# Kernel optimization log

Hardware: AMD Instinct MI355X
Metric: run time of the kernel (lower is better)

The kernel has to match this reference:

```python
import math
import jax, jax.numpy as jnp
import numpy as np

D_MODEL = 768
EXPAND = 2
D_INNER = EXPAND * D_MODEL  # 1536
D_STATE = 16
D_CONV = 4
DT_RANK = math.ceil(D_INNER / 16)  # 96
B, L = 2, 2048
LN_EPS = 1e-5


def setup_inputs() -> dict:
    key = jax.random.key(0)
    ks = jax.random.split(key, 10)
    x = jax.random.normal(ks[0], (B, L, D_MODEL), dtype=jnp.float32)
    ln_g = jnp.ones((D_MODEL,), jnp.float32)
    ln_b = jnp.zeros((D_MODEL,), jnp.float32)
    W_in = jax.random.normal(ks[1], (D_MODEL, 2 * D_INNER), jnp.float32) / np.sqrt(D_MODEL)
    conv_w = jax.random.normal(ks[2], (D_INNER, 1, D_CONV), jnp.float32) / np.sqrt(D_CONV)
    conv_b = jax.random.normal(ks[3], (D_INNER,), jnp.float32) * 0.02
    W_xproj = jax.random.normal(ks[4], (D_INNER, DT_RANK + 2 * D_STATE), jnp.float32) / np.sqrt(D_INNER)
    W_dt = jax.random.normal(ks[5], (DT_RANK, D_INNER), jnp.float32) / np.sqrt(DT_RANK)
    # dt bias init: inverse-softplus of dt ~ LogUniform(1e-3, 1e-1)
    dt = jnp.exp(jax.random.uniform(ks[6], (D_INNER,)) * (math.log(0.1) - math.log(0.001)) + math.log(0.001))
    b_dt = dt + jnp.log(-jnp.expm1(-dt))
    log_A = jnp.log(jnp.tile(jnp.arange(1, D_STATE + 1, dtype=jnp.float32), (D_INNER, 1)))  # (d_inner, N)
    D_param = jnp.ones((D_INNER,), jnp.float32)
    W_out = jax.random.normal(ks[7], (D_INNER, D_MODEL), jnp.float32) / np.sqrt(D_INNER)
    return dict(x=x, ln_g=ln_g, ln_b=ln_b, W_in=W_in, conv_w=conv_w, conv_b=conv_b,
                W_xproj=W_xproj, W_dt=W_dt, b_dt=b_dt, log_A=log_A, D_param=D_param, W_out=W_out)


def _mamba_block(x, ln_g, ln_b, W_in, conv_w, conv_b, W_xproj, W_dt, b_dt, log_A, D_param, W_out):
    residual = x
    # LayerNorm
    mu = jnp.mean(x, axis=-1, keepdims=True)
    var = jnp.var(x, axis=-1, keepdims=True)
    xn = (x - mu) * jax.lax.rsqrt(var + LN_EPS) * ln_g + ln_b
    # in projection -> (u, v)
    uv = xn @ W_in  # (B, L, 2*d_inner)
    u, v = jnp.split(uv, 2, axis=-1)
    # causal depthwise conv1d along length (torch pads both sides then truncates -> left pad only)
    u_c = jnp.transpose(u, (0, 2, 1))  # (B, d_inner, L)
    u_c = jax.lax.conv_general_dilated(
        u_c, conv_w, window_strides=(1,), padding=[(D_CONV - 1, 0)],
        dimension_numbers=('NCH', 'OIH', 'NCH'), feature_group_count=D_INNER)
    u_c = u_c + conv_b[None, :, None]
    u = jnp.transpose(u_c, (0, 2, 1))  # (B, L, d_inner)
    u = jax.nn.silu(u)
    # Selective SSM
    x_dbl = u @ W_xproj  # (B, L, dt_rank + 2N)
    dlt, Bm, Cm = jnp.split(x_dbl, [DT_RANK, DT_RANK + D_STATE], axis=-1)
    delta = jax.nn.softplus(dlt @ W_dt + b_dt)  # (B, L, d_inner)
    A = -jnp.exp(log_A)  # (d_inner, N)
    A_bar = jnp.exp(jnp.einsum('bld,dn->bldn', delta, A))         # discretized A
    Bu = jnp.einsum('bld,bln,bld->bldn', delta, Bm, u)            # B_bar * u
    # parallel scan: h_k = A_bar_k * h_{k-1} + Bu_k
    def comb(e1, e2):
        a1, b1 = e1
        a2, b2 = e2
        return a1 * a2, a2 * b1 + b2
    _, h = jax.lax.associative_scan(comb, (A_bar, Bu), axis=1)
    y = jnp.einsum('bldn,bln->bld', h, Cm) + u * D_param
    # gate + residual
    y = y * jax.nn.silu(v)
    return y @ W_out + residual


def reference(x, ln_g, ln_b, W_in, conv_w, conv_b, W_xproj, W_dt, b_dt, log_A, D_param, W_out):
    return _mamba_block(x, ln_g, ln_b, W_in, conv_w, conv_b, W_xproj, W_dt, b_dt, log_A, D_param, W_out)
```

## Files before the change

kernel.cpp:

```cpp
#include <hip/hip_runtime.h>

#define D_MODEL 768
#define D_INNER 1536
#define D_STATE 16
#define DT_RANK 96
#define BB 2
#define LL 2048
#define TT (BB*LL)
#define NC 64
#define CL 32
#define SKK 4
#define LOG2E 1.44269504f

typedef unsigned short u16;
typedef short bf16x8 __attribute__((ext_vector_type(8)));
typedef unsigned short u16x8 __attribute__((ext_vector_type(8)));
typedef float f32x4  __attribute__((ext_vector_type(4)));

__device__ __forceinline__ float bf2f(u16 u) {
    union { unsigned int i; float f; } c; c.i = ((unsigned int)u) << 16; return c.f;
}
__device__ __forceinline__ u16 f2bf(float f) {
    union { float f; unsigned int i; } c; c.f = f;
    unsigned int x = c.i;
    return (u16)((x + 0x7fffu + ((x >> 16) & 1u)) >> 16);
}
__device__ __forceinline__ float bfu_lo(unsigned int u) {
    union { unsigned int i; float f; } c; c.i = u << 16; return c.f;
}
__device__ __forceinline__ float bfu_hi(unsigned int u) {
    union { unsigned int i; float f; } c; c.i = u & 0xFFFF0000u; return c.f;
}
__device__ __forceinline__ float ldx(const void* p, size_t i, bool f32) {
    return f32 ? ((const float*)p)[i] : bf2f(((const u16*)p)[i]);
}

__device__ __forceinline__ void gload16(const u16* g, u16* l) {
    __builtin_amdgcn_global_load_lds(
        (const __attribute__((address_space(1))) unsigned int*)g,
        (__attribute__((address_space(3))) unsigned int*)l, 16, 0, 0);
}

__device__ __forceinline__ void xcd_swz(int& bx, int& by) {
    const int gx = gridDim.x;
    const int cpx = (gx * gridDim.y) >> 3;
    const int bid = by * gx + bx;
    const int w = (bid & 7) * cpx + (bid >> 3);
    bx = w % gx; by = w / gx;
}

__global__ __launch_bounds__(256) void prep_kernel(
    const void* __restrict__ W_in, const void* __restrict__ W_xp,
    const void* __restrict__ W_dt, const void* __restrict__ W_out,
    u16* __restrict__ WtIn, u16* __restrict__ WtXp,
    u16* __restrict__ WtDt, u16* __restrict__ WtOut,
    const void* __restrict__ x, const void* __restrict__ g,
    const void* __restrict__ b, u16* __restrict__ xn,
    int* __restrict__ flagw)
{
    const int t = threadIdx.x;
    __shared__ int sbad;
    if (t == 0) sbad = 0;
    __syncthreads();
    {
        const u16* px = (const u16*)x;
        int bad = 0;
        for (int i = t; i < 2048; i += 256)
            if (!(fabsf(bf2f(px[2 * i])) < 1e4f)) bad = 1;
        if (bad) atomicOr(&sbad, 1);
    }
    __syncthreads();
    const bool f32 = (sbad != 0);
    int bid = blockIdx.x;
    if (bid == 0 && t == 0) *flagw = sbad;
    if (bid >= 960) {
        const int tok = bid - 960;
        const size_t base = (size_t)tok * D_MODEL;
        float v[3];
        v[0] = ldx(x, base + t, f32);
        v[1] = ldx(x, base + t + 256, f32);
        v[2] = ldx(x, base + t + 512, f32);
        float s = v[0] + v[1] + v[2];
        float q = v[0]*v[0] + v[1]*v[1] + v[2]*v[2];
        #pragma unroll
        for (int o = 32; o > 0; o >>= 1) {
            s += __shfl_down(s, o, 64);
            q += __shfl_down(q, o, 64);
        }
        __shared__ float ss[4], qq[4];
        if ((t & 63) == 0) { ss[t >> 6] = s; qq[t >> 6] = q; }
        __syncthreads();
        const float S = ss[0] + ss[1] + ss[2] + ss[3];
        const float Q = qq[0] + qq[1] + qq[2] + qq[3];
        const float mu  = S * (1.f / D_MODEL);
        const float var = Q * (1.f / D_MODEL) - mu * mu;
        const float rs  = rsqrtf(var + 1e-5f);
        u16* outr = xn + base;
        #pragma unroll
        for (int i = 0; i < 3; ++i) {
            const int c = t + i * 256;
            outr[c] = f2bf((v[i] - mu) * rs * ldx(g, c, f32) + ldx(b, c, f32));
        }
        return;
    }
    const void* src; u16* dst; int K, N, bx, by;
    if (bid < 576)      { src = W_in;  dst = WtIn;  K = 768;  N = 3072; bx = bid % 48; by = bid / 48; }
    else if (bid < 624) { bid -= 576; src = W_xp;  dst = WtXp;  K = 1536; N = 128;  bx = bid % 2;  by = bid / 2; }
    else if (bid < 672) { bid -= 624; src = W_dt;  dst = WtDt;  K = 96;   N = 1536; bx = bid % 24; by = bid / 24; }
    else                { bid -= 672; src = W_out; dst = WtOut; K = 1536; N = 768;  bx = bid % 12; by = bid / 12; }
    __shared__ u16 tile[64][72];
    const int n0 = bx * 64, k0 = by * 64;
    {
        const int r = t >> 2, c = (t & 3) * 16;
        const int k = k0 + r;
        if (k < K) {
            if (f32) {
                const float* sp = (const float*)src + (size_t)k * N + n0 + c;
                #pragma unroll
                for (int q = 0; q < 4; ++q) {
                    const float4 v = *(const float4*)(sp + 4 * q);
                    tile[r][c + 4*q + 0] = f2bf(v.x);
                    tile[r][c + 4*q + 1] = f2bf(v.y);
                    tile[r][c + 4*q + 2] = f2bf(v.z);
                    tile[r][c + 4*q + 3] = f2bf(v.w);
                }
            } else {
                const u16* sp = (const u16*)src + (size_t)k * N + n0 + c;
                *(u16x8*)(&tile[r][c])     = *(const u16x8*)(sp);
                *(u16x8*)(&tile[r][c + 8]) = *(const u16x8*)(sp + 8);
            }
        }
    }
    __syncthreads();
    {
        const int nl = t >> 2, kl = (t & 3) * 16;
        const int n = n0 + nl;
        if (k0 + kl < K) {
            u16x8 t0, t1;
            #pragma unroll
            for (int i = 0; i < 8; ++i) t0[i] = tile[kl + i][nl];
            #pragma unroll
            for (int i = 0; i < 8; ++i) t1[i] = tile[kl + 8 + i][nl];
            u16* dp = dst + (size_t)n * K + k0 + kl;
            *(u16x8*)(dp)     = t0;
            *(u16x8*)(dp + 8) = t1;
        }
    }
}

template<int EPI, int BK>
__global__ __launch_bounds__(256) void mfma_gemm(
    const u16* __restrict__ A, const u16* __restrict__ Bt,
    u16* __restrict__ C, void* __restrict__ Cout, const void* __restrict__ aux,
    float* __restrict__ Cf, const int* __restrict__ flagp,
    int Kslice, int lda, int ldbt, int ldc)
{
    const bool f32 = (*flagp != 0);
    __shared__ alignas(16) u16 As[3 * 64 * BK];
    __shared__ alignas(16) u16 Bs[3 * 64 * BK];
    const int tid  = threadIdx.x;
    const int wave = tid >> 6, lane = tid & 63;
    const int lrow = lane & 15, quad = lane >> 4;
    int bx = blockIdx.x, by = blockIdx.y;
    if (gridDim.z == 1) xcd_swz(bx, by);
    const int row0 = by * 64, col0 = bx * 64;
    const int k0   = blockIdx.z * Kslice;
    constexpr int LPR = BK / 8;
    constexpr int PM  = LPR - 1;
    constexpr int RPO = 64 / LPR;
    constexpr int NOP = BK / 32;
    constexpr int V1  = 2 * NOP;
    constexpr int V2  = 4 * NOP;
    const int srow = lane / LPR;
    const int pc   = (lane % LPR) ^ (srow & PM);
    const int skk  = pc * 8;
    const int wb   = wave * 16 * BK;
    const u16* gA = A  + (size_t)(row0 + wave * 16 + srow) * lda  + k0 + skk;
    const u16* gB = Bt + (size_t)(col0 + wave * 16 + srow) * ldbt + k0 + skk;
    const int nst = Kslice / BK;
    constexpr int BUF = 64 * BK;
    #pragma unroll
    for (int o = 0; o < NOP; ++o) {
        gload16(gA + (size_t)o * RPO * lda,  &As[wb + o * 512]);
        gload16(gB + (size_t)o * RPO * ldbt, &Bs[wb + o * 512]);
    }
    if (nst > 1) {
        #pragma unroll
        for (int o = 0; o < NOP; ++o) {
            gload16(gA + BK + (size_t)o * RPO * lda,  &As[BUF + wb + o * 512]);
            gload16(gB + BK + (size_t)o * RPO * ldbt, &Bs[BUF + wb + o * 512]);
        }
    }
    f32x4 acc[4] = {{0.f,0.f,0.f,0.f},{0.f,0.f,0.f,0.f},{0.f,0.f,0.f,0.f},{0.f,0.f,0.f,0.f}};
    const int sw = (lrow & PM) << 3;
    int cur = 0, nxt2 = 2;
    for (int t = 0; t < nst; ++t) {
        if (t + 2 < nst) {
            const int kt = (t + 2) * BK;
            const int poff = nxt2 * BUF;
            #pragma unroll
            for (int o = 0; o < NOP; ++o) {
                gload16(gA + kt + (size_t)o * RPO * lda,  &As[poff + wb + o * 512]);
                gload16(gB + kt + (size_t)o * RPO * ldbt, &Bs[poff + wb + o * 512]);
            }
            asm volatile("s_waitcnt vmcnt(%0)" :: "i"(V2) : "memory");
        } else if (t + 1 < nst) {
            asm volatile("s_waitcnt vmcnt(%0)" :: "i"(V1) : "memory");
        } else {
            asm volatile("s_waitcnt vmcnt(0)" ::: "memory");
        }
        __builtin_amdgcn_s_barrier();
        asm volatile("" ::: "memory");
        const int boff = cur * BUF;
        #pragma unroll
        for (int kk = 0; kk < NOP; ++kk) {
            const bf16x8 af = *(const bf16x8*)(
                &As[boff + (wave * 16 + lrow) * BK + ((kk * 32 + quad * 8) ^ sw)]);
            #pragma unroll
            for (int q = 0; q < 4; ++q) {
                const bf16x8 bq = *(const bf16x8*)(
                    &Bs[boff + (q * 16 + lrow) * BK + ((kk * 32 + quad * 8) ^ sw)]);
                acc[q] = __builtin_amdgcn_mfma_f32_16x16x32_bf16(af, bq, acc[q], 0, 0, 0);
            }
        }
        __builtin_amdgcn_s_barrier();
        asm volatile("" ::: "memory");
        cur = (cur == 2) ? 0 : cur + 1;
        nxt2 = (nxt2 == 2) ? 0 : nxt2 + 1;
    }
    #pragma unroll
    for (int t = 0; t < 4; ++t) {
        #pragma unroll
        for (int r = 0; r < 4; ++r) {
            const int row = row0 + wave * 16 + quad * 4 + r;
            const int col = col0 + t * 16 + lrow;
            const size_t idx = (size_t)row * ldc + col;
            float vv = acc[t][r];
            if (EPI == 1) {
                vv += ldx(aux, col, f32);
                vv = (vv > 20.f) ? vv : log1pf(__expf(vv));
                C[idx] = f2bf(vv);
            } else if (EPI == 2) {
                vv += ldx(aux, idx, f32);
                if (f32) ((float*)Cout)[idx] = vv;
                else     ((u16*)Cout)[idx]   = f2bf(vv);
            } else if (EPI == 3) {
                Cf[(size_t)blockIdx.z * (TT * 128) + idx] = vv;
            } else {
                C[idx] = f2bf(vv);
            }
        }
    }
}

template<int EPI>
__global__ __launch_bounds__(256) void mfma_gemm128(
    const u16* __restrict__ A, const u16* __restrict__ Bt,
    u16* __restrict__ C, void* __restrict__ Cout, const void* __restrict__ aux,
    const int* __restrict__ flagp,
    int K, int lda, int ldbt, int ldc)
{
    const bool f32 = (*flagp != 0);
    __shared__ alignas(16) u16 As[3 * 128 * 32];
    __shared__ alignas(16) u16 Bs[3 * 128 * 32];
    const int tid  = threadIdx.x;
    const int wave = tid >> 6, lane = tid & 63;
    const int lrow = lane & 15, quad = lane >> 4;
    const int wy = wave >> 1, wx = wave & 1;
    int bx = blockIdx.x, by = blockIdx.y;
    if (gridDim.z == 1) xcd_swz(bx, by);
    const int row0 = by * 128, col0 = bx * 128;
    const int srw = lane >> 2;
    const int pc  = (lane & 3) ^ (srw & 3);
    const int skk = pc * 8;
    const int r0 = wave * 16 + srw;
    const int r1 = r0 + 64;
    const int wb0 = wave * 512, wb1 = (wave + 4) * 512;
    const u16* gA0 = A  + (size_t)(row0 + r0) * lda  + skk;
    const u16* gA1 = A  + (size_t)(row0 + r1) * lda  + skk;
    const u16* gB0 = Bt + (size_t)(col0 + r0) * ldbt + skk;
    const u16* gB1 = Bt + (size_t)(col0 + r1) * ldbt + skk;
    const int nst = K >> 5;
    constexpr int BUF = 128 * 32;
    gload16(gA0, &As[wb0]); gload16(gA1, &As[wb1]);
    gload16(gB0, &Bs[wb0]); gload16(gB1, &Bs[wb1]);
    if (nst > 1) {
        gload16(gA0 + 32, &As[BUF + wb0]); gload16(gA1 + 32, &As[BUF + wb1]);
        gload16(gB0 + 32, &Bs[BUF + wb0]); gload16(gB1 + 32, &Bs[BUF + wb1]);
    }
    f32x4 acc[4][4];
    #pragma unroll
    for (int i = 0; i < 4; ++i)
        #pragma unroll
        for (int j = 0; j < 4; ++j) acc[i][j] = (f32x4){0.f,0.f,0.f,0.f};
    const int sw = (lrow & 3) << 3;
    int cur = 0, nxt2 = 2;
    for (int t = 0; t < nst; ++t) {
        if (t + 2 < nst) {
            const int kt = (t + 2) * 32;
            const int poff = nxt2 * BUF;
            gload16(gA0 + kt, &As[poff + wb0]); gload16(gA1 + kt, &As[poff + wb1]);
            gload16(gB0 + kt, &Bs[poff + wb0]); gload16(gB1 + kt, &Bs[poff + wb1]);
            asm volatile("s_waitcnt vmcnt(8)" ::: "memory");
        } else if (t + 1 < nst) {
            asm volatile("s_waitcnt vmcnt(4)" ::: "memory");
        } else {
            asm volatile("s_waitcnt vmcnt(0)" ::: "memory");
        }
        __builtin_amdgcn_s_barrier();
        asm volatile("" ::: "memory");
        const int boff = cur * BUF;
        bf16x8 af[4], bf_[4];
        #pragma unroll
        for (int i = 0; i < 4; ++i)
            af[i] = *(const bf16x8*)(
                &As[boff + (wy * 64 + i * 16 + lrow) * 32 + ((quad * 8) ^ sw)]);
        #pragma unroll
        for (int j = 0; j < 4; ++j)
            bf_[j] = *(const bf16x8*)(
                &Bs[boff + (wx * 64 + j * 16 + lrow) * 32 + ((quad * 8) ^ sw)]);
        #pragma unroll
        for (int i = 0; i < 4; ++i)
            #pragma unroll
            for (int j = 0; j < 4; ++j)
                acc[i][j] = __builtin_amdgcn_mfma_f32_16x16x32_bf16(af[i], bf_[j], acc[i][j], 0, 0, 0);
        __builtin_amdgcn_s_barrier();
        asm volatile("" ::: "memory");
        cur = (cur == 2) ? 0 : cur + 1;
        nxt2 = (nxt2 == 2) ? 0 : nxt2 + 1;
    }
    #pragma unroll
    for (int i = 0; i < 4; ++i) {
        #pragma unroll
        for (int j = 0; j < 4; ++j) {
            #pragma unroll
            for (int r = 0; r < 4; ++r) {
                const int row = row0 + wy * 64 + i * 16 + quad * 4 + r;
                const int col = col0 + wx * 64 + j * 16 + lrow;
                const size_t idx = (size_t)row * ldc + col;
                float vv = acc[i][j][r];
                if (EPI == 1) {
                    vv += ldx(aux, col, f32);
                    vv = (vv > 20.f) ? vv : log1pf(__expf(vv));
                    C[idx] = f2bf(vv);
                } else if (EPI == 2) {
                    vv += ldx(aux, idx, f32);
                    if (f32) ((float*)Cout)[idx] = vv;
                    else     ((u16*)Cout)[idx]   = f2bf(vv);
                } else {
                    C[idx] = f2bf(vv);
                }
            }
        }
    }
}

__global__ __launch_bounds__(256) void convert_kernel(const float* __restrict__ src,
                                                      u16* __restrict__ dst, int n)
{
    const int i = blockIdx.x * 256 + threadIdx.x;
    if (i < n)
        dst[i] = f2bf(src[i] + src[i + TT*128] + src[i + 2*TT*128] + src[i + 3*TT*128]);
}

__global__ __launch_bounds__(256) void conv_silu_kernel(
    const u16* __restrict__ uv, const void* __restrict__ cw, const void* __restrict__ cb,
    u16* __restrict__ us, const int* __restrict__ flagp)
{
    const bool f32 = (*flagp != 0);
    const int gid = blockIdx.x * 256 + threadIdx.x;
    const int nd8 = D_INNER / 8;
    const int d8  = gid % nd8;
    const int tok = gid / nd8;
    const int d   = d8 * 8;
    const int l   = tok & (LL - 1);
    float acc[8], w[4][8];
    #pragma unroll
    for (int i = 0; i < 8; ++i) acc[i] = ldx(cb, d + i, f32);
    #pragma unroll
    for (int i = 0; i < 8; ++i) {
        if (f32) {
            const float4 wv = *(const float4*)((const float*)cw + (size_t)(d + i) * 4);
            w[0][i] = wv.x; w[1][i] = wv.y; w[2][i] = wv.z; w[3][i] = wv.w;
        } else {
            const u16* wp = (const u16*)cw + (size_t)(d + i) * 4;
            w[0][i] = bf2f(wp[0]); w[1][i] = bf2f(wp[1]);
            w[2][i] = bf2f(wp[2]); w[3][i] = bf2f(wp[3]);
        }
    }
    #pragma unroll
    for (int j = 0; j < 4; ++j) {
        if (l - 3 + j >= 0) {
            const u16x8 uvv = *(const u16x8*)(&uv[(size_t)(tok - 3 + j) * (2 * D_INNER) + d]);
            #pragma unroll
            for (int i = 0; i < 8; ++i) acc[i] += bf2f(uvv[i]) * w[j][i];
        }
    }
    u16x8 o;
    #pragma unroll
    for (int i = 0; i < 8; ++i) o[i] = f2bf(acc[i] / (1.f + __expf(-acc[i])));
    *(u16x8*)(&us[(size_t)tok * D_INNER + d]) = o;
}

__global__ __launch_bounds__(256) void scan1_kernel(
    const u16* __restrict__ delta, const u16* __restrict__ us,
    const u16* __restrict__ xdbl, const void* __restrict__ log_A,
    float* __restrict__ carrySD, float* __restrict__ carryH,
    const int* __restrict__ flagp)
{
    const bool f32 = (*flagp != 0);
    const int d = blockIdx.x * 256 + threadIdx.x;
    const int c = blockIdx.y, b = blockIdx.z;
    float A2[16], h[16];
    #pragma unroll
    for (int j = 0; j < 16; ++j) {
        A2[j] = -__expf(ldx(log_A, d * D_STATE + j, f32)) * LOG2E;
        h[j] = 0.f;
    }
    bool pw = true;
    #pragma unroll
    for (int j = 1; j < 16; ++j)
        pw = pw && (fabsf(A2[j] - (j + 1) * A2[0]) <= 0.02f * (j + 1) * fabsf(A2[0]));
    float sdl = 0.f;
    size_t tok = (size_t)b * LL + c * CL;
    if (pw) {
        #pragma unroll 2
        for (int t = 0; t < CL; ++t, ++tok) {
            const float dl = bf2f(delta[tok * D_INNER + d]);
            const float ul = bf2f(us[tok * D_INNER + d]);
            const uint4 B0 = *(const uint4*)(xdbl + tok * 128 + DT_RANK);
            const uint4 B1 = *(const uint4*)(xdbl + tok * 128 + DT_RANK + 8);
            const float dlul = dl * ul;
            sdl += dl;
            const unsigned int bw[8] = {B0.x,B0.y,B0.z,B0.w,B1.x,B1.y,B1.z,B1.w};
            const float a1 = exp2f(dl * A2[0]);
            float aj = 1.f;
            #pragma unroll
            for (int j = 0; j < 16; ++j) {
                aj *= a1;
                const float Bn = (j & 1) ? bfu_hi(bw[j >> 1]) : bfu_lo(bw[j >> 1]);
                h[j] = aj * h[j] + dlul * Bn;
            }
        }
    } else {
        #pragma unroll 2
        for (int t = 0; t < CL; ++t, ++tok) {
            const float dl = bf2f(delta[tok * D_INNER + d]);
            const float ul = bf2f(us[tok * D_INNER + d]);
            const uint4 B0 = *(const uint4*)(xdbl + tok * 128 + DT_RANK);
            const uint4 B1 = *(const uint4*)(xdbl + tok * 128 + DT_RANK + 8);
            const float dlul = dl * ul;
            sdl += dl;
            const unsigned int bw[8] = {B0.x,B0.y,B0.z,B0.w,B1.x,B1.y,B1.z,B1.w};
            #pragma unroll
            for (int j = 0; j < 16; ++j) {
                const float Bn = (j & 1) ? bfu_hi(bw[j >> 1]) : bfu_lo(bw[j >> 1]);
                h[j] = exp2f(dl * A2[j]) * h[j] + dlul * Bn;
            }
        }
    }
    const size_t cc = (size_t)b * NC + c;
    carrySD[cc * D_INNER + d] = sdl;
    const size_t ci = cc * (D_INNER * D_STATE) + d;
    #pragma unroll
    for (int j = 0; j < 16; ++j)
        carryH[ci + (size_t)j * D_INNER] = h[j];
}

__global__ __launch_bounds__(256) void scan2_kernel(
    const float* __restrict__ carrySD, float* __restrict__ carryH,
    const void* __restrict__ log_A, const int* __restrict__ flagp)
{
    const bool f32 = (*flagp != 0);
    const int gid = blockIdx.x * 256 + threadIdx.x;
    const int b   = gid / (D_INNER * D_STATE);
    const int dn  = gid % (D_INNER * D_STATE);
    const int j   = dn / D_INNER, d = dn % D_INNER;
    const float A2j = -__expf(ldx(log_A, d * D_STATE + j, f32)) * LOG2E;
    float hrun = 0.f;
    #pragma unroll 4
    for (int c = 0; c < NC; ++c) {
        const size_t cc = (size_t)b * NC + c;
        const float sdl = carrySD[cc * D_INNER + d];
        const size_t ci = cc * (D_INNER * D_STATE) + dn;
        const float hh = carryH[ci];
        carryH[ci] = hrun;
        hrun = exp2f(A2j * sdl) * hrun + hh;
    }
}

__global__ __launch_bounds__(256) void scan3_kernel(
    const u16* __restrict__ delta, const u16* __restrict__ us,
    const u16* __restrict__ xdbl, u16* __restrict__ uv,
    const void* __restrict__ log_A, const void* __restrict__ D_param,
    const float* __restrict__ carryH, const int* __restrict__ flagp)
{
    const bool f32 = (*flagp != 0);
    const int d = blockIdx.x * 256 + threadIdx.x;
    const int c = blockIdx.y, b = blockIdx.z;
    const float Dd = ldx(D_param, d, f32);
    float A2[16], h[16];
    const size_t ci = ((size_t)b * NC + c) * (D_INNER * D_STATE) + d;
    #pragma unroll
    for (int j = 0; j < 16; ++j)
        A2[j] = -__expf(ldx(log_A, d * D_STATE + j, f32)) * LOG2E;
    bool pw = true;
    #pragma unroll
    for (int j = 1; j < 16; ++j)
        pw = pw && (fabsf(A2[j] - (j + 1) * A2[0]) <= 0.02f * (j + 1) * fabsf(A2[0]));
    #pragma unroll
    for (int j = 0; j < 16; ++j)
        h[j] = carryH[ci + (size_t)j * D_INNER];
    size_t tok = (size_t)b * LL + c * CL;
    if (pw) {
        #pragma unroll 2
        for (int t = 0; t < CL; ++t, ++tok) {
            const float dl = bf2f(delta[tok * D_INNER + d]);
            const float ul = bf2f(us[tok * D_INNER + d]);
            const uint4 B0 = *(const uint4*)(xdbl + tok * 128 + DT_RANK);
            const uint4 B1 = *(const uint4*)(xdbl + tok * 128 + DT_RANK + 8);
            const uint4 C0 = *(const uint4*)(xdbl + tok * 128 + DT_RANK + D_STATE);
            const uint4 C1 = *(const uint4*)(xdbl + tok * 128 + DT_RANK + D_STATE + 8);
            const float dlul = dl * ul;
            const unsigned int bw[8] = {B0.x,B0.y,B0.z,B0.w,B1.x,B1.y,B1.z,B1.w};
            const unsigned int cw_[8] = {C0.x,C0.y,C0.z,C0.w,C1.x,C1.y,C1.z,C1.w};
            const float a1 = exp2f(dl * A2[0]);
            float aj = 1.f, p = 0.f;
            #pragma unroll
            for (int j = 0; j < 16; ++j) {
                aj *= a1;
                const float Bn = (j & 1) ? bfu_hi(bw[j >> 1]) : bfu_lo(bw[j >> 1]);
                const float Cn = (j & 1) ? bfu_hi(cw_[j >> 1]) : bfu_lo(cw_[j >> 1]);
                h[j] = aj * h[j] + dlul * Bn;
                p += h[j] * Cn;
            }
            const float vv = bf2f(uv[tok * (2*D_INNER) + D_INNER + d]);
            uv[tok * (2*D_INNER) + d] = f2bf((p + ul * Dd) * (vv / (1.f + __expf(-vv))));
        }
    } else {
        #pragma unroll 2
        for (int t = 0; t < CL; ++t, ++tok) {
            const float dl = bf2f(delta[tok * D_INNER + d]);
            const float ul = bf2f(us[tok * D_INNER + d]);
            const uint4 B0 = *(const uint4*)(xdbl + tok * 128 + DT_RANK);
            const uint4 B1 = *(const uint4*)(xdbl + tok * 128 + DT_RANK + 8);
            const uint4 C0 = *(const uint4*)(xdbl + tok * 128 + DT_RANK + D_STATE);
            const uint4 C1 = *(const uint4*)(xdbl + tok * 128 + DT_RANK + D_STATE + 8);
            const float dlul = dl * ul;
            const unsigned int bw[8] = {B0.x,B0.y,B0.z,B0.w,B1.x,B1.y,B1.z,B1.w};
            const unsigned int cw_[8] = {C0.x,C0.y,C0.z,C0.w,C1.x,C1.y,C1.z,C1.w};
            float p = 0.f;
            #pragma unroll
            for (int j = 0; j < 16; ++j) {
                const float Bn = (j & 1) ? bfu_hi(bw[j >> 1]) : bfu_lo(bw[j >> 1]);
                const float Cn = (j & 1) ? bfu_hi(cw_[j >> 1]) : bfu_lo(cw_[j >> 1]);
                h[j] = exp2f(dl * A2[j]) * h[j] + dlul * Bn;
                p += h[j] * Cn;
            }
            const float vv = bf2f(uv[tok * (2*D_INNER) + D_INNER + d]);
            uv[tok * (2*D_INNER) + d] = f2bf((p + ul * Dd) * (vv / (1.f + __expf(-vv))));
        }
    }
}

extern "C" void kernel_launch(void* const* d_in, const int* in_sizes, int n_in,
                              void* d_out, int out_size, void* d_ws, size_t ws_size,
                              hipStream_t stream)
{
    const void* x      = d_in[0];
    const void* ln_g   = d_in[1];
    const void* ln_b   = d_in[2];
    const void* W_in   = d_in[3];
    const void* conv_w = d_in[4];
    const void* conv_b = d_in[5];
    const void* W_xp   = d_in[6];
    const void* W_dt   = d_in[7];
    const void* b_dt   = d_in[8];
    const void* log_A  = d_in[9];
    const void* D_par  = d_in[10];
    const void* W_out  = d_in[11];

    int* flag  = (int*)d_ws;
    u16* ws    = (u16*)((char*)d_ws + 512);
    u16* xn    = ws;
    u16* uv    = xn + (size_t)TT * D_MODEL;
    u16* us    = uv + (size_t)TT * 2 * D_INNER;
    u16* xdbl  = us + (size_t)TT * D_INNER;
    u16* delta = xdbl + (size_t)TT * 128;
    float* carryH  = (float*)(delta + (size_t)TT * D_INNER);
    float* carrySD = carryH + (size_t)BB * NC * D_INNER * D_STATE;
    u16* WtIn  = (u16*)(carrySD + (size_t)BB * NC * D_INNER);
    u16* WtXp  = WtIn  + (size_t)2 * D_INNER * D_MODEL;
    u16* WtDt  = WtXp  + (size_t)(DT_RANK + 2 * D_STATE) * D_INNER;
    u16* WtOut = WtDt  + (size_t)D_INNER * DT_RANK;
    float* xdblF = (float*)(WtOut + (size_t)D_MODEL * D_INNER);

    prep_kernel<<<960 + TT, 256, 0, stream>>>(
        W_in, W_xp, W_dt, W_out, WtIn, WtXp, WtDt, WtOut,
        x, ln_g, ln_b, xn, flag);
    mfma_gemm128<0><<<dim3(2 * D_INNER / 128, TT / 128), 256, 0, stream>>>(
        xn, WtIn, uv, nullptr, nullptr, flag, D_MODEL, D_MODEL, D_MODEL, 2 * D_INNER);
    conv_silu_kernel<<<(TT * D_INNER / 8) / 256, 256, 0, stream>>>(uv, conv_w, conv_b, us, flag);
    mfma_gemm<3, 64><<<dim3(2, TT / 64, SKK), 256, 0, stream>>>(
        us, WtXp, nullptr, nullptr, nullptr, xdblF, flag,
        D_INNER / SKK, D_INNER, D_INNER, 128);
    convert_kernel<<<(TT * 128 + 255) / 256, 256, 0, stream>>>(xdblF, xdbl, TT * 128);
    mfma_gemm<1, 32><<<dim3(D_INNER / 64, TT / 64, 1), 256, 0, stream>>>(
        xdbl, WtDt, delta, nullptr, b_dt, nullptr, flag,
        DT_RANK, 128, DT_RANK, D_INNER);
    scan1_kernel<<<dim3(D_INNER / 256, NC, BB), 256, 0, stream>>>(
        delta, us, xdbl, log_A, carrySD, carryH, flag);
    scan2_kernel<<<(BB * D_INNER * D_STATE) / 256, 256, 0, stream>>>(
        carrySD, carryH, log_A, flag);
    scan3_kernel<<<dim3(D_INNER / 256, NC, BB), 256, 0, stream>>>(
        delta, us, xdbl, uv, log_A, D_par, carryH, flag);
    mfma_gemm<2, 64><<<dim3(D_MODEL / 64, TT / 64, 1), 256, 0, stream>>>(
        uv, WtOut, nullptr, d_out, x, nullptr, flag,
        D_INNER, 2 * D_INNER, D_INNER, D_MODEL);
}
```

Baseline: 280.3 us.

## Drop split-K for x_proj GEMM and fold chunk carry scan into scan3

Replaces the split-K x_proj GEMM plus fp32 reduction kernel with a single-pass GEMM writing bf16 directly. It also removes the separate inter-chunk carry kernel: each scan3 thread now recomputes its incoming state by iterating over all earlier chunks. This saves two launches and an fp32 round-trip through memory. In exchange, the GEMM grid is much smaller, and the carry recomputation is quadratic in chunk count with redundant exp2 work.

Measured after the change: 317.7 us. 1.13x slower.

```diff
diff --git a/kernel.cpp b/kernel.cpp
--- a/kernel.cpp
+++ b/kernel.cpp
@@ -9,7 +9,6 @@
 #define TT (BB*LL)
 #define NC 64
 #define CL 32
-#define SKK 4
 #define LOG2E 1.44269504f
 
 typedef unsigned short u16;
@@ -152,7 +151,7 @@
 __global__ __launch_bounds__(256) void mfma_gemm(
     const u16* __restrict__ A, const u16* __restrict__ Bt,
     u16* __restrict__ C, void* __restrict__ Cout, const void* __restrict__ aux,
-    float* __restrict__ Cf, const int* __restrict__ flagp,
+    const int* __restrict__ flagp,
     int Kslice, int lda, int ldbt, int ldc)
 {
     const bool f32 = (*flagp != 0);
@@ -162,9 +161,8 @@
     const int wave = tid >> 6, lane = tid & 63;
     const int lrow = lane & 15, quad = lane >> 4;
     int bx = blockIdx.x, by = blockIdx.y;
-    if (gridDim.z == 1) xcd_swz(bx, by);
+    xcd_swz(bx, by);
     const int row0 = by * 64, col0 = bx * 64;
-    const int k0   = blockIdx.z * Kslice;
     constexpr int LPR = BK / 8;
     constexpr int PM  = LPR - 1;
     constexpr int RPO = 64 / LPR;
@@ -175,8 +173,8 @@
     const int pc   = (lane % LPR) ^ (srow & PM);
     const int skk  = pc * 8;
     const int wb   = wave * 16 * BK;
-    const u16* gA = A  + (size_t)(row0 + wave * 16 + srow) * lda  + k0 + skk;
-    const u16* gB = Bt + (size_t)(col0 + wave * 16 + srow) * ldbt + k0 + skk;
+    const u16* gA = A  + (size_t)(row0 + wave * 16 + srow) * lda  + skk;
+    const u16* gB = Bt + (size_t)(col0 + wave * 16 + srow) * ldbt + skk;
     const int nst = Kslice / BK;
     constexpr int BUF = 64 * BK;
     #pragma unroll
@@ -244,8 +242,6 @@
                 vv += ldx(aux, idx, f32);
                 if (f32) ((float*)Cout)[idx] = vv;
                 else     ((u16*)Cout)[idx]   = f2bf(vv);
-            } else if (EPI == 3) {
-                Cf[(size_t)blockIdx.z * (TT * 128) + idx] = vv;
             } else {
                 C[idx] = f2bf(vv);
             }
@@ -268,7 +264,7 @@
     const int lrow = lane & 15, quad = lane >> 4;
     const int wy = wave >> 1, wx = wave & 1;
     int bx = blockIdx.x, by = blockIdx.y;
-    if (gridDim.z == 1) xcd_swz(bx, by);
+    xcd_swz(bx, by);
     const int row0 = by * 128, col0 = bx * 128;
     const int srw = lane >> 2;
     const int pc  = (lane & 3) ^ (srw & 3);
@@ -338,29 +334,10 @@
                 const int row = row0 + wy * 64 + i * 16 + quad * 4 + r;
                 const int col = col0 + wx * 64 + j * 16 + lrow;
                 const size_t idx = (size_t)row * ldc + col;
-                float vv = acc[i][j][r];
-                if (EPI == 1) {
-                    vv += ldx(aux, col, f32);
-                    vv = (vv > 20.f) ? vv : log1pf(__expf(vv));
-                    C[idx] = f2bf(vv);
-                } else if (EPI == 2) {
-                    vv += ldx(aux, idx, f32);
-                    if (f32) ((float*)Cout)[idx] = vv;
-                    else     ((u16*)Cout)[idx]   = f2bf(vv);
-                } else {
-                    C[idx] = f2bf(vv);
-                }
-            }
-        }
-    }
-}
-
-__global__ __launch_bounds__(256) void convert_kernel(const float* __restrict__ src,
-                                                      u16* __restrict__ dst, int n)
-{
-    const int i = blockIdx.x * 256 + threadIdx.x;
-    if (i < n)
-        dst[i] = f2bf(src[i] + src[i + TT*128] + src[i + 2*TT*128] + src[i + 3*TT*128]);
+                C[idx] = f2bf(acc[i][j][r]);
+            }
+        }
+    }
 }
 
 __global__ __launch_bounds__(256) void conv_silu_kernel(
@@ -467,50 +444,35 @@
         carryH[ci + (size_t)j * D_INNER] = h[j];
 }
 
-__global__ __launch_bounds__(256) void scan2_kernel(
-    const float* __restrict__ carrySD, float* __restrict__ carryH,
-    const void* __restrict__ log_A, const int* __restrict__ flagp)
-{
-    const bool f32 = (*flagp != 0);
-    const int gid = blockIdx.x * 256 + threadIdx.x;
-    const int b   = gid / (D_INNER * D_STATE);
-    const int dn  = gid % (D_INNER * D_STATE);
-    const int j   = dn / D_INNER, d = dn % D_INNER;
-    const float A2j = -__expf(ldx(log_A, d * D_STATE + j, f32)) * LOG2E;
-    float hrun = 0.f;
-    #pragma unroll 4
-    for (int c = 0; c < NC; ++c) {
-        const size_t cc = (size_t)b * NC + c;
-        const float sdl = carrySD[cc * D_INNER + d];
-        const size_t ci = cc * (D_INNER * D_STATE) + dn;
-        const float hh = carryH[ci];
-        carryH[ci] = hrun;
-        hrun = exp2f(A2j * sdl) * hrun + hh;
-    }
-}
-
 __global__ __launch_bounds__(256) void scan3_kernel(
     const u16* __restrict__ delta, const u16* __restrict__ us,
     const u16* __restrict__ xdbl, u16* __restrict__ uv,
     const void* __restrict__ log_A, const void* __restrict__ D_param,
-    const float* __restrict__ carryH, const int* __restrict__ flagp)
+    const float* __restrict__ carrySD, const float* __restrict__ carryH,
+    const int* __restrict__ flagp)
 {
     const bool f32 = (*flagp != 0);
     const int d = blockIdx.x * 256 + threadIdx.x;
     const int c = blockIdx.y, b = blockIdx.z;
     const float Dd = ldx(D_param, d, f32);
     float A2[16], h[16];
-    const size_t ci = ((size_t)b * NC + c) * (D_INNER * D_STATE) + d;
-    #pragma unroll
-    for (int j = 0; j < 16; ++j)
+    #pragma unroll
+    for (int j = 0; j < 16; ++j) {
         A2[j] = -__expf(ldx(log_A, d * D_STATE + j, f32)) * LOG2E;
+        h[j] = 0.f;
+    }
     bool pw = true;
     #pragma unroll
     for (int j = 1; j < 16; ++j)
         pw = pw && (fabsf(A2[j] - (j + 1) * A2[0]) <= 0.02f * (j + 1) * fabsf(A2[0]));
-    #pragma unroll
-    for (int j = 0; j < 16; ++j)
-        h[j] = carryH[ci + (size_t)j * D_INNER];
+    for (int cp = 0; cp < c; ++cp) {
+        const size_t cc = (size_t)b * NC + cp;
+        const float sdl = carrySD[cc * D_INNER + d];
+        const float* hp = carryH + cc * (D_INNER * D_STATE) + d;
+        #pragma unroll
+        for (int j = 0; j < 16; ++j)
+            h[j] = exp2f(A2[j] * sdl) * h[j] + hp[(size_t)j * D_INNER];
+    }
     size_t tok = (size_t)b * LL + c * CL;
     if (pw) {
         #pragma unroll 2
@@ -593,7 +555,6 @@
     u16* WtXp  = WtIn  + (size_t)2 * D_INNER * D_MODEL;
     u16* WtDt  = WtXp  + (size_t)(DT_RANK + 2 * D_STATE) * D_INNER;
     u16* WtOut = WtDt  + (size_t)D_INNER * DT_RANK;
-    float* xdblF = (float*)(WtOut + (size_t)D_MODEL * D_INNER);
 
     prep_kernel<<<960 + TT, 256, 0, stream>>>(
         W_in, W_xp, W_dt, W_out, WtIn, WtXp, WtDt, WtOut,
@@ -601,20 +562,17 @@
     mfma_gemm128<0><<<dim3(2 * D_INNER / 128, TT / 128), 256, 0, stream>>>(
         xn, WtIn, uv, nullptr, nullptr, flag, D_MODEL, D_MODEL, D_MODEL, 2 * D_INNER);
     conv_silu_kernel<<<(TT * D_INNER / 8) / 256, 256, 0, stream>>>(uv, conv_w, conv_b, us, flag);
-    mfma_gemm<3, 64><<<dim3(2, TT / 64, SKK), 256, 0, stream>>>(
-        us, WtXp, nullptr, nullptr, nullptr, xdblF, flag,
-        D_INNER / SKK, D_INNER, D_INNER, 128);
-    convert_kernel<<<(TT * 128 + 255) / 256, 256, 0, stream>>>(xdblF, xdbl, TT * 128);
+    mfma_gemm<0, 64><<<dim3(2, TT / 64, 1), 256, 0, stream>>>(
+        us, WtXp, xdbl, nullptr, nullptr, flag,
+        D_INNER, D_INNER, D_INNER, 128);
     mfma_gemm<1, 32><<<dim3(D_INNER / 64, TT / 64, 1), 256, 0, stream>>>(
-        xdbl, WtDt, delta, nullptr, b_dt, nullptr, flag,
+        xdbl, WtDt, delta, nullptr, b_dt, flag,
         DT_RANK, 128, DT_RANK, D_INNER);
     scan1_kernel<<<dim3(D_INNER / 256, NC, BB), 256, 0, stream>>>(
         delta, us, xdbl, log_A, carrySD, carryH, flag);
-    scan2_kernel<<<(BB * D_INNER * D_STATE) / 256, 256, 0, stream>>>(
-        carrySD, carryH, log_A, flag);
     scan3_kernel<<<dim3(D_INNER / 256, NC, BB), 256, 0, stream>>>(
-        delta, us, xdbl, uv, log_A, D_par, carryH, flag);
+        delta, us, xdbl, uv, log_A, D_par, carrySD, carryH, flag);
     mfma_gemm<2, 64><<<dim3(D_MODEL / 64, TT / 64, 1), 256, 0, stream>>>(
-        uv, WtOut, nullptr, d_out, x, nullptr, flag,
+        uv, WtOut, nullptr, d_out, x, flag,
         D_INNER, 2 * D_INNER, D_INNER, D_MODEL);
 }
```
